# Performance work log

Measured on AMD Instinct MI355X. Metric: run time of the kernel, lower is better.

## Reference

```python
import jax, jax.numpy as jnp
import numpy as np

N, E = 4096, 131072
IN_DIM, HID, OUT_DIM = 128, 64, 128
H1 = 4                       # gat1 heads
D_MODEL = HID * H1           # 256
NHEAD = 4
D_FF = 2048


def setup_inputs() -> dict:
    key = jax.random.key(0)
    ks = jax.random.split(key, 16)
    def w(k, shape, scale=0.05):
        return jax.random.normal(k, shape, dtype=jnp.float32) * scale
    return {
        "x": jax.random.normal(ks[0], (N, IN_DIM), dtype=jnp.float32),
        "edge_index": jax.random.randint(ks[1], (2, E), 0, N, dtype=jnp.int32),
        "gat1_w": w(ks[2], (H1 * HID, IN_DIM)),
        "gat1_asrc": w(ks[3], (H1, HID)),
        "gat1_adst": w(ks[4], (H1, HID)),
        "gat1_b": jnp.zeros((H1 * HID,), jnp.float32),
        "in_proj_w": w(ks[5], (3 * D_MODEL, D_MODEL)),
        "in_proj_b": jnp.zeros((3 * D_MODEL,), jnp.float32),
        "out_proj_w": w(ks[6], (D_MODEL, D_MODEL)),
        "out_proj_b": jnp.zeros((D_MODEL,), jnp.float32),
        "lin1_w": w(ks[7], (D_FF, D_MODEL)),
        "lin1_b": jnp.zeros((D_FF,), jnp.float32),
        "lin2_w": w(ks[8], (D_MODEL, D_FF)),
        "lin2_b": jnp.zeros((D_MODEL,), jnp.float32),
        "ln1_g": jnp.ones((D_MODEL,), jnp.float32),
        "ln1_b": jnp.zeros((D_MODEL,), jnp.float32),
        "ln2_g": jnp.ones((D_MODEL,), jnp.float32),
        "ln2_b": jnp.zeros((D_MODEL,), jnp.float32),
        "gat2_w": w(ks[9], (OUT_DIM, D_MODEL)),
        "gat2_asrc": w(ks[10], (1, OUT_DIM)),
        "gat2_adst": w(ks[11], (1, OUT_DIM)),
        "gat2_b": jnp.zeros((OUT_DIM,), jnp.float32),
    }


def _add_self_loops(ei, n):
    loops = jnp.arange(n, dtype=ei.dtype)
    return jnp.concatenate([ei, jnp.stack([loops, loops])], axis=1)


def _segment_softmax(logits, seg, n):
    # numerically stable softmax over edges grouped by destination node
    m = jax.ops.segment_max(logits, seg, num_segments=n)
    m = jnp.where(jnp.isfinite(m), m, 0.0)
    e = jnp.exp(logits - m[seg])
    s = jax.ops.segment_sum(e, seg, num_segments=n)
    return e / (s[seg] + 1e-16)


def _gat(x, ei, W, asrc, adst, b, heads, out_ch):
    n = x.shape[0]
    h = (x @ W.T).reshape(n, heads, out_ch)          # [N,H,C]
    al_s = jnp.einsum('nhc,hc->nh', h, asrc)
    al_d = jnp.einsum('nhc,hc->nh', h, adst)
    src, dst = ei[0], ei[1]
    logits = jax.nn.leaky_relu(al_s[src] + al_d[dst], 0.2)   # [E,H]
    alpha = _segment_softmax(logits, dst, n)
    out = jax.ops.segment_sum(h[src] * alpha[:, :, None], dst, num_segments=n)
    return out.reshape(n, heads * out_ch) + b


def _ln(x, g, b):
    mu = x.mean(-1, keepdims=True)
    v = x.var(-1, keepdims=True)
    return (x - mu) / jnp.sqrt(v + 1e-5) * g + b


def _forward(x, edge_index, gat1_w, gat1_asrc, gat1_adst, gat1_b,
             in_proj_w, in_proj_b, out_proj_w, out_proj_b,
             lin1_w, lin1_b, lin2_w, lin2_b, ln1_g, ln1_b, ln2_g, ln2_b,
             gat2_w, gat2_asrc, gat2_adst, gat2_b):
    n = x.shape[0]
    ei = _add_self_loops(edge_index, n)
    h = jax.nn.elu(_gat(x, ei, gat1_w, gat1_asrc, gat1_adst, gat1_b, H1, HID))  # [N, 256]
    # TransformerEncoderLayer (post-norm, relu, no dropout in eval)
    hd = D_MODEL // NHEAD
    qkv = h @ in_proj_w.T + in_proj_b
    q, k, v = jnp.split(qkv, 3, axis=-1)
    q = q.reshape(n, NHEAD, hd)
    k = k.reshape(n, NHEAD, hd)
    v = v.reshape(n, NHEAD, hd)
    scores = jnp.einsum('qhd,khd->hqk', q, k) / jnp.sqrt(jnp.float32(hd))
    attn = jax.nn.softmax(scores, axis=-1)
    o = jnp.einsum('hqk,khd->qhd', attn, v).reshape(n, D_MODEL)
    o = o @ out_proj_w.T + out_proj_b
    h = _ln(h + o, ln1_g, ln1_b)
    ff = jax.nn.relu(h @ lin1_w.T + lin1_b) @ lin2_w.T + lin2_b
    h = _ln(h + ff, ln2_g, ln2_b)
    return _gat(h, ei, gat2_w, gat2_asrc, gat2_adst, gat2_b, 1, OUT_DIM)


def reference(x, edge_index, gat1_w, gat1_asrc, gat1_adst, gat1_b,
              in_proj_w, in_proj_b, out_proj_w, out_proj_b,
              lin1_w, lin1_b, lin2_w, lin2_b, ln1_g, ln1_b, ln2_g, ln2_b,
              gat2_w, gat2_asrc, gat2_adst, gat2_b):
    return _forward(x, edge_index, gat1_w, gat1_asrc, gat1_adst, gat1_b,
                    in_proj_w, in_proj_b, out_proj_w, out_proj_b,
                    lin1_w, lin1_b, lin2_w, lin2_b, ln1_g, ln1_b, ln2_g, ln2_b,
                    gat2_w, gat2_asrc, gat2_adst, gat2_b)
```

## Files before the change

kernel.cpp:

```cpp
#include <hip/hip_runtime.h>
#include <hip/hip_bf16.h>
#include <math.h>

#define NN 4096
#define NE 131072
#define EE (NE + NN)

typedef unsigned short u16;
typedef short s8v __attribute__((ext_vector_type(8)));
typedef float f4v __attribute__((ext_vector_type(4)));
typedef float f16v __attribute__((ext_vector_type(16)));

__device__ inline u16 f2b(float f) {
  __hip_bfloat16 h = __float2bfloat16(f);
  return __builtin_bit_cast(u16, h);
}
__device__ inline float b2f(u16 v) {
  unsigned int u = ((unsigned int)v) << 16;
  return __builtin_bit_cast(float, u);
}

__global__ void k_count(const int* __restrict__ ei, int* __restrict__ deg) {
  int e = blockIdx.x * 256 + threadIdx.x;
  if (e >= EE) return;
  int dst = (e < NE) ? ei[NE + e] : (e - NE);
  atomicAdd(&deg[dst], 1);
}

__global__ __launch_bounds__(1024) void k_scan(const int* __restrict__ deg, int* __restrict__ rowptr) {
  __shared__ int lds[1024];
  int t = threadIdx.x;
  int v0 = deg[t*4+0], v1 = deg[t*4+1], v2 = deg[t*4+2], v3 = deg[t*4+3];
  int s1 = v0+v1, s2 = s1+v2, s3 = s2+v3;
  lds[t] = s3;
  __syncthreads();
  for (int off = 1; off < 1024; off <<= 1) {
    int add = (t >= off) ? lds[t-off] : 0;
    __syncthreads();
    lds[t] += add;
    __syncthreads();
  }
  int base = lds[t] - s3;
  rowptr[t*4+1] = base + v0;
  rowptr[t*4+2] = base + s1;
  rowptr[t*4+3] = base + s2;
  rowptr[t*4+4] = base + s3;
  if (t == 0) rowptr[0] = 0;
}

__global__ void k_scatter(const int* __restrict__ ei, const int* __restrict__ rowptr,
                          int* __restrict__ cursor, int* __restrict__ csr_src) {
  int e = blockIdx.x * 256 + threadIdx.x;
  if (e >= EE) return;
  int src, dst;
  if (e < NE) { src = ei[e]; dst = ei[NE + e]; }
  else { src = e - NE; dst = src; }
  int pos = rowptr[dst] + atomicAdd(&cursor[dst], 1);
  csr_src[pos] = src;
}

__global__ __launch_bounds__(256) void k_f2b_all(
    const float* a0, u16* b0, int e0, const float* a1, u16* b1, int e1,
    const float* a2, u16* b2, int e2, const float* a3, u16* b3, int e3,
    const float* a4, u16* b4, int e4, const float* a5, u16* b5, int e5,
    const float* a6, u16* b6, int e6)
{
  int i = blockIdx.x * 256 + threadIdx.x;
  const float* s; u16* d; int base;
  if      (i < e0) { s=a0; d=b0; base=0;  }
  else if (i < e1) { s=a1; d=b1; base=e0; }
  else if (i < e2) { s=a2; d=b2; base=e1; }
  else if (i < e3) { s=a3; d=b3; base=e2; }
  else if (i < e4) { s=a4; d=b4; base=e3; }
  else if (i < e5) { s=a5; d=b5; base=e4; }
  else if (i < e6) { s=a6; d=b6; base=e5; }
  else return;
  int j = i - base;
  float4 v = ((const float4*)s)[j];
  u16 r[4] = {f2b(v.x), f2b(v.y), f2b(v.z), f2b(v.w)};
  *(uint2*)(d + (size_t)j*4) = *(uint2*)r;
}

template<int HEADS, int C>
__global__ __launch_bounds__(256) void k_alogits(
    const u16* __restrict__ featb, const float* __restrict__ asrc,
    const float* __restrict__ adst, float* __restrict__ als, float* __restrict__ ald)
{
  constexpr int F = HEADS * C;
  int n = blockIdx.x, t = threadIdx.x;
  float f = b2f(featb[(size_t)n*F + t]);
  float ps = f * asrc[t];
  float pd = f * adst[t];
  #pragma unroll
  for (int off = 32; off; off >>= 1) {
    ps += __shfl_xor(ps, off);
    pd += __shfl_xor(pd, off);
  }
  if constexpr (C == 64) {
    if ((t & 63) == 0) {
      int hh = t >> 6;
      als[(size_t)n*HEADS + hh] = ps;
      ald[(size_t)n*HEADS + hh] = pd;
    }
  } else {
    __shared__ float sh[2][2];
    if ((t & 63) == 0) { sh[t>>6][0] = ps; sh[t>>6][1] = pd; }
    __syncthreads();
    if (t == 0) {
      als[n] = sh[0][0] + sh[1][0];
      ald[n] = sh[0][1] + sh[1][1];
    }
  }
}

template<int HEADS, int C, bool DO_ELU, bool WB>
__global__ __launch_bounds__(256) void k_gat_agg(
    const u16* __restrict__ featb, const float* __restrict__ als,
    const float* __restrict__ ald, const float* __restrict__ bias,
    const int* __restrict__ rowptr, const int* __restrict__ csr_src,
    float* __restrict__ out, u16* __restrict__ outb)
{
  constexpr int F = HEADS * C;
  int n = blockIdx.x, t = threadIdx.x;
  __shared__ float m_sh[HEADS], s_sh[HEADS];
  __shared__ float alpha_sh[HEADS][64];
  __shared__ int src_sh[64];
  int start = rowptr[n];
  int deg = rowptr[n+1] - start;
  int lane = t & 63, wv = t >> 6;
  for (int hh = wv; hh < HEADS; hh += F/64) {
    float adl = ald[(size_t)n*HEADS + hh];
    float mx = -INFINITY;
    for (int i = lane; i < deg; i += 64) {
      int s = csr_src[start + i];
      float lg = als[(size_t)s*HEADS + hh] + adl;
      lg = (lg > 0.f) ? lg : 0.2f * lg;
      mx = fmaxf(mx, lg);
    }
    #pragma unroll
    for (int off = 32; off; off >>= 1) mx = fmaxf(mx, __shfl_xor(mx, off));
    float sm = 0.f;
    for (int i = lane; i < deg; i += 64) {
      int s = csr_src[start + i];
      float lg = als[(size_t)s*HEADS + hh] + adl;
      lg = (lg > 0.f) ? lg : 0.2f * lg;
      sm += expf(lg - mx);
    }
    #pragma unroll
    for (int off = 32; off; off >>= 1) sm += __shfl_xor(sm, off);
    if (lane == 0) { m_sh[hh] = mx; s_sh[hh] = sm; }
  }
  __syncthreads();
  int hh = t / C;
  int hh2 = t >> 6;
  int ia = t & 63;
  float acc0 = 0.f, acc1 = 0.f;
  for (int c0 = 0; c0 < deg; c0 += 64) {
    int cn = min(64, deg - c0);
    if (hh2 < HEADS && ia < cn) {
      int s = csr_src[start + c0 + ia];
      if (hh2 == 0) src_sh[ia] = s;
      float lg = als[(size_t)s*HEADS + hh2] + ald[(size_t)n*HEADS + hh2];
      lg = (lg > 0.f) ? lg : 0.2f * lg;
      alpha_sh[hh2][ia] = expf(lg - m_sh[hh2]);
    }
    __syncthreads();
    int i = 0;
    for (; i + 1 < cn; i += 2) {
      int s0 = src_sh[i], s1 = src_sh[i+1];
      float a0 = alpha_sh[hh][i], a1 = alpha_sh[hh][i+1];
      acc0 += a0 * b2f(featb[(size_t)s0*F + t]);
      acc1 += a1 * b2f(featb[(size_t)s1*F + t]);
    }
    if (i < cn)
      acc0 += alpha_sh[hh][i] * b2f(featb[(size_t)src_sh[i]*F + t]);
    __syncthreads();
  }
  float o = (acc0 + acc1) / (s_sh[hh] + 1e-16f) + bias[t];
  if (DO_ELU) o = (o > 0.f) ? o : (expf(o) - 1.f);
  out[(size_t)n*F + t] = o;
  if (WB) outb[(size_t)n*F + t] = f2b(o);
}

template<int MODE>
__global__ __launch_bounds__(256) void k_gemm_mfma(
    const u16* __restrict__ A, const u16* __restrict__ B,
    const float* __restrict__ bias, float* __restrict__ Cf, u16* __restrict__ Cb,
    u16* __restrict__ Qb, u16* __restrict__ Kb, u16* __restrict__ Vt,
    int M, int N, int K)
{
  __shared__ u16 Al[64*64];
  __shared__ u16 Bl[64*64];
  char* Ab = (char*)Al;
  char* Bb = (char*)Bl;
  const int t = threadIdx.x;
  const int lane = t & 63;
  const int lr = lane & 15, lk = lane >> 4;
  const int wid = t >> 6;
  const int wm = wid & 1, wn = wid >> 1;
  const int m0 = blockIdx.y * 64, n0 = blockIdx.x * 64;

  f4v acc[2][2];
  #pragma unroll
  for (int mi = 0; mi < 2; ++mi)
    #pragma unroll
    for (int ni = 0; ni < 2; ++ni)
      acc[mi][ni] = f4v{0.f, 0.f, 0.f, 0.f};

  for (int k0 = 0; k0 < K; k0 += 64) {
    #pragma unroll
    for (int i = 0; i < 2; ++i) {
      int idx = t + i*256;
      int row = idx >> 3, ch = idx & 7;
      s8v av = *(const s8v*)(A + (size_t)(m0 + row)*K + k0 + ch*8);
      *(s8v*)(Ab + row*128 + ((ch*16) ^ ((row & 7) << 4))) = av;
      s8v bv = *(const s8v*)(B + (size_t)(n0 + row)*K + k0 + ch*8);
      *(s8v*)(Bb + row*128 + ((ch*16) ^ ((row & 7) << 4))) = bv;
    }
    __syncthreads();
    #pragma unroll
    for (int ks = 0; ks < 2; ++ks) {
      s8v af[2], bfr[2];
      #pragma unroll
      for (int mi = 0; mi < 2; ++mi) {
        int row = wm*32 + mi*16 + lr;
        int ch = ks*4 + lk;
        af[mi] = *(const s8v*)(Ab + row*128 + ((ch*16) ^ ((row & 7) << 4)));
      }
      #pragma unroll
      for (int ni = 0; ni < 2; ++ni) {
        int row = wn*32 + ni*16 + lr;
        int ch = ks*4 + lk;
        bfr[ni] = *(const s8v*)(Bb + row*128 + ((ch*16) ^ ((row & 7) << 4)));
      }
      #pragma unroll
      for (int mi = 0; mi < 2; ++mi)
        #pragma unroll
        for (int ni = 0; ni < 2; ++ni)
          acc[mi][ni] = __builtin_amdgcn_mfma_f32_16x16x32_bf16(af[mi], bfr[ni], acc[mi][ni], 0, 0, 0);
    }
    __syncthreads();
  }
  #pragma unroll
  for (int ni = 0; ni < 2; ++ni) {
    int col = n0 + wn*32 + ni*16 + lr;
    float bc = bias ? bias[col] : 0.f;
    #pragma unroll
    for (int mi = 0; mi < 2; ++mi) {
      int row0 = m0 + wm*32 + mi*16 + lk*4;
      float v[4];
      #pragma unroll
      for (int r = 0; r < 4; ++r) v[r] = acc[mi][ni][r] + bc;
      if (MODE == 0) {
        #pragma unroll
        for (int r = 0; r < 4; ++r) Cf[(size_t)(row0 + r)*N + col] = v[r];
      } else if (MODE == 2) {
        #pragma unroll
        for (int r = 0; r < 4; ++r) Cb[(size_t)(row0 + r)*N + col] = f2b(v[r]);
      } else {
        if (col < 512) {
          int head = (col >> 6) & 3;
          int d = col & 63;
          u16* dst = ((col < 256) ? Qb : Kb) + (size_t)head*262144 + d;
          #pragma unroll
          for (int r = 0; r < 4; ++r) dst[(size_t)(row0 + r)*64] = f2b(v[r]);
        } else {
          int cc = col - 512;
          int head = cc >> 6;
          int d = cc & 63;
          int quad = row0 & 12;
          int qs = (quad == 4) ? 8 : ((quad == 8) ? 4 : quad);
          size_t nphys = (size_t)((row0 & ~15) | qs);
          u16 o4[4];
          #pragma unroll
          for (int r = 0; r < 4; ++r) o4[r] = f2b(v[r]);
          *(uint2*)(Vt + (size_t)head*262144 + (size_t)d*4096 + nphys) = *(uint2*)o4;
        }
      }
    }
  }
}

template<int MODE>
__global__ __launch_bounds__(256) void k_gemm2(
    const u16* __restrict__ A, const u16* __restrict__ B,
    const float* __restrict__ bias, float* __restrict__ Cf, u16* __restrict__ Cb,
    int M, int N, int K, int ksl)
{
  __shared__ u16 Al[128*64];
  __shared__ u16 Bl[64*64];
  char* Ab = (char*)Al;
  char* Bb = (char*)Bl;
  const int t = threadIdx.x;
  const int lane = t & 63;
  const int lr = lane & 15, lk = lane >> 4;
  const int wv = t >> 6;
  const int m0 = blockIdx.y * 128, n0 = blockIdx.x * 64;
  const int z = blockIdx.z;
  const int kbeg = z * ksl, kend = kbeg + ksl;

  f4v acc[2][4];
  #pragma unroll
  for (int mi = 0; mi < 2; ++mi)
    #pragma unroll
    for (int ni = 0; ni < 4; ++ni)
      acc[mi][ni] = f4v{0.f, 0.f, 0.f, 0.f};

  for (int k0 = kbeg; k0 < kend; k0 += 64) {
    #pragma unroll
    for (int i = 0; i < 4; ++i) {
      int idx = t + i*256;
      int row = idx >> 3, ch = idx & 7;
      s8v av = *(const s8v*)(A + (size_t)(m0 + row)*K + k0 + ch*8);
      *(s8v*)(Ab + row*128 + ((ch*16) ^ ((row & 7) << 4))) = av;
    }
    #pragma unroll
    for (int i = 0; i < 2; ++i) {
      int idx = t + i*256;
      int row = idx >> 3, ch = idx & 7;
      s8v bv = *(const s8v*)(B + (size_t)(n0 + row)*K + k0 + ch*8);
      *(s8v*)(Bb + row*128 + ((ch*16) ^ ((row & 7) << 4))) = bv;
    }
    __syncthreads();
    #pragma unroll
    for (int ks = 0; ks < 2; ++ks) {
      s8v af[2], bfr[4];
      #pragma unroll
      for (int mi = 0; mi < 2; ++mi) {
        int row = wv*32 + mi*16 + lr;
        int ch = ks*4 + lk;
        af[mi] = *(const s8v*)(Ab + row*128 + ((ch*16) ^ ((row & 7) << 4)));
      }
      #pragma unroll
      for (int ni = 0; ni < 4; ++ni) {
        int row = ni*16 + lr;
        int ch = ks*4 + lk;
        bfr[ni] = *(const s8v*)(Bb + row*128 + ((ch*16) ^ ((row & 7) << 4)));
      }
      #pragma unroll
      for (int mi = 0; mi < 2; ++mi)
        #pragma unroll
        for (int ni = 0; ni < 4; ++ni)
          acc[mi][ni] = __builtin_amdgcn_mfma_f32_16x16x32_bf16(af[mi], bfr[ni], acc[mi][ni], 0, 0, 0);
    }
    __syncthreads();
  }
  #pragma unroll
  for (int ni = 0; ni < 4; ++ni) {
    int col = n0 + ni*16 + lr;
    float bc = (MODE == 4) ? 0.f : bias[col];
    #pragma unroll
    for (int mi = 0; mi < 2; ++mi) {
      int row0 = m0 + wv*32 + mi*16 + lk*4;
      #pragma unroll
      for (int r = 0; r < 4; ++r) {
        float v = acc[mi][ni][r] + bc;
        if (MODE == 1) {
          v = fmaxf(v, 0.f);
          Cb[(size_t)(row0 + r)*N + col] = f2b(v);
        } else {
          (Cf + (size_t)z*M*N)[(size_t)(row0 + r)*N + col] = v;
        }
      }
    }
  }
}

template<bool WB>
__global__ __launch_bounds__(256) void k_ln(
    const float* __restrict__ a, const float* __restrict__ res,
    const float* __restrict__ g, const float* __restrict__ bb,
    float* __restrict__ out, u16* __restrict__ outb)
{
  int n = blockIdx.x, t = threadIdx.x;
  __shared__ float part[4];
  float v = a[(size_t)n*256 + t] + res[(size_t)n*256 + t];
  float s = v;
  #pragma unroll
  for (int off = 32; off; off >>= 1) s += __shfl_xor(s, off);
  if ((t & 63) == 0) part[t >> 6] = s;
  __syncthreads();
  float mean = (part[0] + part[1] + part[2] + part[3]) * (1.f/256.f);
  __syncthreads();
  float d = v - mean;
  float s2 = d * d;
  #pragma unroll
  for (int off = 32; off; off >>= 1) s2 += __shfl_xor(s2, off);
  if ((t & 63) == 0) part[t >> 6] = s2;
  __syncthreads();
  float var = (part[0] + part[1] + part[2] + part[3]) * (1.f/256.f);
  float rstd = rsqrtf(var + 1e-5f);
  float o = d * rstd * g[t] + bb[t];
  out[(size_t)n*256 + t] = o;
  if (WB) outb[(size_t)n*256 + t] = f2b(o);
}

template<bool WB>
__global__ __launch_bounds__(256) void k_ln_sk(
    const float* __restrict__ Po, const float* __restrict__ bias,
    const float* __restrict__ res, const float* __restrict__ g,
    const float* __restrict__ bb, float* __restrict__ out, u16* __restrict__ outb)
{
  int n = blockIdx.x, t = threadIdx.x;
  __shared__ float part[4];
  const size_t MN = (size_t)NN * 256;
  size_t idx = (size_t)n*256 + t;
  float v = Po[idx] + Po[MN + idx] + Po[2*MN + idx] + Po[3*MN + idx]
          + bias[t] + res[idx];
  float s = v;
  #pragma unroll
  for (int off = 32; off; off >>= 1) s += __shfl_xor(s, off);
  if ((t & 63) == 0) part[t >> 6] = s;
  __syncthreads();
  float mean = (part[0] + part[1] + part[2] + part[3]) * (1.f/256.f);
  __syncthreads();
  float d = v - mean;
  float s2 = d * d;
  #pragma unroll
  for (int off = 32; off; off >>= 1) s2 += __shfl_xor(s2, off);
  if ((t & 63) == 0) part[t >> 6] = s2;
  __syncthreads();
  float var = (part[0] + part[1] + part[2] + part[3]) * (1.f/256.f);
  float rstd = rsqrtf(var + 1e-5f);
  float o = d * rstd * g[t] + bb[t];
  out[idx] = o;
  if (WB) outb[idx] = f2b(o);
}

__global__ __launch_bounds__(512) void k_attn2(
    const u16* __restrict__ Qb, const u16* __restrict__ Kb,
    const u16* __restrict__ Vt, float* __restrict__ op,
    float* __restrict__ mb, float* __restrict__ lb)
{
  const int strip = blockIdx.x;
  const int head  = blockIdx.y;
  const int z     = blockIdx.z;
  const int q0 = strip * 32;
  const int t = threadIdx.x;
  const int s = t >> 6;
  const int l = t & 63;
  const int lq = l & 31;
  const int lh = l >> 5;

  __shared__ float lds_O[4][32][68];
  __shared__ float lds_m[4][32];
  __shared__ float lds_l[4][32];

  const u16* Qh = Qb + (size_t)head * (4096*64);
  const u16* Kh = Kb + (size_t)head * (4096*64);
  const u16* Vh = Vt + (size_t)head * (64*4096);

  s8v qf[4];
#pragma unroll
  for (int dc = 0; dc < 4; ++dc)
    qf[dc] = *(const s8v*)(Qh + (size_t)(q0 + lq)*64 + dc*16 + lh*8);

  f16v accO[2];
#pragma unroll
  for (int dm = 0; dm < 2; ++dm)
#pragma unroll
    for (int i = 0; i < 16; ++i) accO[dm][i] = 0.f;

  float mrow = -INFINITY, lrow = 0.f;
  const float CE = 0.18033688011112042f;

  const int kt0 = z * 2048 + s * 256;
  for (int kt = kt0; kt < kt0 + 256; kt += 64) {
    f16v st[2];
#pragma unroll
    for (int c = 0; c < 2; ++c)
#pragma unroll
      for (int i = 0; i < 16; ++i) st[c][i] = 0.f;
#pragma unroll
    for (int dc = 0; dc < 4; ++dc) {
      s8v kf0 = *(const s8v*)(Kh + (size_t)(kt + lq)*64 + dc*16 + lh*8);
      s8v kf1 = *(const s8v*)(Kh + (size_t)(kt + 32 + lq)*64 + dc*16 + lh*8);
      st[0] = __builtin_amdgcn_mfma_f32_32x32x16_bf16(kf0, qf[dc], st[0], 0, 0, 0);
      st[1] = __builtin_amdgcn_mfma_f32_32x32x16_bf16(kf1, qf[dc], st[1], 0, 0, 0);
    }
    float mx = st[0][0];
#pragma unroll
    for (int i = 1; i < 16; ++i) mx = fmaxf(mx, st[0][i]);
#pragma unroll
    for (int i = 0; i < 16; ++i) mx = fmaxf(mx, st[1][i]);
    mx = fmaxf(mx, __shfl_xor(mx, 32));
    float mn = fmaxf(mrow, mx);
    float sc = exp2f((mrow - mn) * CE);
    mrow = mn;
    float ps = 0.f;
#pragma unroll
    for (int c = 0; c < 2; ++c)
#pragma unroll
      for (int i = 0; i < 16; ++i) {
        float p = exp2f((st[c][i] - mn) * CE);
        st[c][i] = p;
        ps += p;
      }
    ps += __shfl_xor(ps, 32);
    lrow = lrow * sc + ps;
#pragma unroll
    for (int dm = 0; dm < 2; ++dm)
#pragma unroll
      for (int i = 0; i < 16; ++i) accO[dm][i] *= sc;

#pragma unroll
    for (int c = 0; c < 2; ++c) {
#pragma unroll
      for (int kc = 0; kc < 2; ++kc) {
        union { s8v v; unsigned int w[4]; } pb;
#pragma unroll
        for (int wd = 0; wd < 4; ++wd) {
          u16 lo16 = f2b(st[c][kc*8 + wd*2]);
          u16 hi16 = f2b(st[c][kc*8 + wd*2 + 1]);
          pb.w[wd] = (unsigned int)lo16 | ((unsigned int)hi16 << 16);
        }
#pragma unroll
        for (int dm = 0; dm < 2; ++dm) {
          s8v vf = *(const s8v*)(Vh + (size_t)(dm*32 + lq)*4096 + kt + c*32 + kc*16 + lh*8);
          accO[dm] = __builtin_amdgcn_mfma_f32_32x32x16_bf16(vf, pb.v, accO[dm], 0, 0, 0);
        }
      }
    }
  }

#pragma unroll
  for (int lev = 0; lev < 3; ++lev) {
    const int step = 1 << lev;
    __syncthreads();
    if ((s & (2*step - 1)) == step) {
      int slot = (s - step) >> (lev + 1);
      if (l < 32) { lds_m[slot][lq] = mrow; lds_l[slot][lq] = lrow; }
#pragma unroll
      for (int dm = 0; dm < 2; ++dm)
#pragma unroll
        for (int g = 0; g < 4; ++g) {
          f4v v;
#pragma unroll
          for (int rr = 0; rr < 4; ++rr) v[rr] = accO[dm][g*4 + rr];
          *(f4v*)&lds_O[slot][lq][dm*32 + lh*4 + g*8] = v;
        }
    }
    __syncthreads();
    if ((s & (2*step - 1)) == 0) {
      int slot = s >> (lev + 1);
      float mp = lds_m[slot][lq], lp = lds_l[slot][lq];
      float M = fmaxf(mrow, mp);
      float w0 = exp2f((mrow - M) * CE);
      float w1 = exp2f((mp - M) * CE);
      lrow = lrow * w0 + lp * w1;
      mrow = M;
#pragma unroll
      for (int dm = 0; dm < 2; ++dm)
#pragma unroll
        for (int g = 0; g < 4; ++g) {
          f4v vp = *(const f4v*)&lds_O[slot][lq][dm*32 + lh*4 + g*8];
#pragma unroll
          for (int rr = 0; rr < 4; ++rr)
            accO[dm][g*4 + rr] = accO[dm][g*4 + rr] * w0 + vp[rr] * w1;
        }
    }
  }

  if (s == 0) {
    int pb = (z*4 + head)*128 + strip;
    if (l < 32) { mb[pb*32 + lq] = mrow; lb[pb*32 + lq] = lrow; }
#pragma unroll
    for (int dm = 0; dm < 2; ++dm)
#pragma unroll
      for (int g = 0; g < 4; ++g) {
        f4v v;
#pragma unroll
        for (int rr = 0; rr < 4; ++rr) v[rr] = accO[dm][g*4 + rr];
        *(f4v*)&op[(size_t)pb*2048 + lq*64 + dm*32 + lh*4 + g*8] = v;
      }
  }
}

__global__ __launch_bounds__(256) void k_attn_mrg(
    const float* __restrict__ op, const float* __restrict__ mb,
    const float* __restrict__ lb, u16* __restrict__ attno_b)
{
  const int strip = blockIdx.x;
  const int head = blockIdx.y;
  const int t = threadIdx.x;
  const int q = t >> 3;
  const int d0 = (t & 7) * 8;
  const float CE = 0.18033688011112042f;
  int p0 = (0*4 + head)*128 + strip;
  int p1 = (1*4 + head)*128 + strip;
  float m0 = mb[p0*32 + q], m1 = mb[p1*32 + q];
  float M = fmaxf(m0, m1);
  float w0 = exp2f((m0 - M) * CE);
  float w1 = exp2f((m1 - M) * CE);
  float L = w0 * lb[p0*32 + q] + w1 * lb[p1*32 + q];
  float inv = 1.f / L;
  const float* o0 = op + (size_t)p0*2048 + q*64 + d0;
  const float* o1 = op + (size_t)p1*2048 + q*64 + d0;
  u16 o8[8];
#pragma unroll
  for (int i = 0; i < 8; ++i)
    o8[i] = f2b((w0 * o0[i] + w1 * o1[i]) * inv);
  *(uint4*)(attno_b + (size_t)(strip*32 + q)*256 + head*64 + d0) = *(uint4*)o8;
}

extern "C" void kernel_launch(void* const* d_in, const int* in_sizes, int n_in,
                              void* d_out, int out_size, void* d_ws, size_t ws_size,
                              hipStream_t stream)
{
  const float* x       = (const float*)d_in[0];
  const int*   ei      = (const int*)d_in[1];
  const float* gat1_w  = (const float*)d_in[2];
  const float* gat1_as = (const float*)d_in[3];
  const float* gat1_ad = (const float*)d_in[4];
  const float* gat1_b  = (const float*)d_in[5];
  const float* inp_w   = (const float*)d_in[6];
  const float* inp_b   = (const float*)d_in[7];
  const float* outp_w  = (const float*)d_in[8];
  const float* outp_b  = (const float*)d_in[9];
  const float* lin1_w  = (const float*)d_in[10];
  const float* lin1_b  = (const float*)d_in[11];
  const float* lin2_w  = (const float*)d_in[12];
  const float* lin2_b  = (const float*)d_in[13];
  const float* ln1_g   = (const float*)d_in[14];
  const float* ln1_bb  = (const float*)d_in[15];
  const float* ln2_g   = (const float*)d_in[16];
  const float* ln2_bb  = (const float*)d_in[17];
  const float* gat2_w  = (const float*)d_in[18];
  const float* gat2_as = (const float*)d_in[19];
  const float* gat2_ad = (const float*)d_in[20];
  const float* gat2_b  = (const float*)d_in[21];
  float* out = (float*)d_out;
  (void)in_sizes; (void)n_in; (void)out_size; (void)ws_size;

  char* ws = (char*)d_ws;
  size_t off = 0;
  auto nxt = [&](size_t bytes) { size_t r = off; off += (bytes + 255) & ~(size_t)255; return r; };
  int* deg      = (int*)(ws + nxt((size_t)NN*4));
  int* cursor   = (int*)(ws + nxt((size_t)NN*4));
  int* rowptr   = (int*)(ws + nxt((size_t)(NN+1)*4));
  int* csr_src  = (int*)(ws + nxt((size_t)EE*4));
  float* al1s   = (float*)(ws + nxt((size_t)NN*4*4));
  float* al1d   = (float*)(ws + nxt((size_t)NN*4*4));
  float* hgat1  = (float*)(ws + nxt((size_t)NN*256*4));
  float* tmp256 = (float*)(ws + nxt((size_t)NN*256*4));
  float* hln1   = (float*)(ws + nxt((size_t)NN*256*4));
  float* hln2   = (float*)(ws + nxt((size_t)NN*256*4));
  float* Po     = (float*)(ws + nxt((size_t)4*NN*256*4));
  float* al2s   = (float*)(ws + nxt((size_t)NN*4));
  float* al2d   = (float*)(ws + nxt((size_t)NN*4));
  u16* x_b      = (u16*)(ws + nxt((size_t)NN*128*2));
  u16* feat1_b  = (u16*)(ws + nxt((size_t)NN*256*2));
  u16* feat2_b  = (u16*)(ws + nxt((size_t)NN*128*2));
  u16* hgat1_b  = (u16*)(ws + nxt((size_t)NN*256*2));
  u16* attno_b  = (u16*)(ws + nxt((size_t)NN*256*2));
  u16* hln1_b   = (u16*)(ws + nxt((size_t)NN*256*2));
  u16* hln2_b   = (u16*)(ws + nxt((size_t)NN*256*2));
  u16* ff1_b    = (u16*)(ws + nxt((size_t)NN*2048*2));
  u16* Qb       = (u16*)(ws + nxt((size_t)4*4096*64*2));
  u16* Kb       = (u16*)(ws + nxt((size_t)4*4096*64*2));
  u16* Vt       = (u16*)(ws + nxt((size_t)4*4096*64*2));
  u16* inp_w_b  = (u16*)(ws + nxt((size_t)768*256*2));
  u16* outp_w_b = (u16*)(ws + nxt((size_t)256*256*2));
  u16* lin1_w_b = (u16*)(ws + nxt((size_t)2048*256*2));
  u16* lin2_w_b = (u16*)(ws + nxt((size_t)256*2048*2));
  u16* gat1_w_b = (u16*)(ws + nxt((size_t)256*128*2));
  u16* gat2_w_b = (u16*)(ws + nxt((size_t)128*256*2));

  float* a_op = Po;
  float* a_mb = Po + (size_t)1024*2048;
  float* a_lb = a_mb + 32768;

  hipMemsetAsync(deg, 0, (size_t)NN*4, stream);
  hipMemsetAsync(cursor, 0, (size_t)NN*4, stream);
  k_count<<<(EE+255)/256, 256, 0, stream>>>(ei, deg);
  k_scan<<<1, 1024, 0, stream>>>(deg, rowptr);
  k_scatter<<<(EE+255)/256, 256, 0, stream>>>(ei, rowptr, cursor, csr_src);

  k_f2b_all<<<1856, 256, 0, stream>>>(
      inp_w,  inp_w_b,  49152,
      outp_w, outp_w_b, 65536,
      lin1_w, lin1_w_b, 196608,
      lin2_w, lin2_w_b, 327680,
      gat1_w, gat1_w_b, 335872,
      gat2_w, gat2_w_b, 344064,
      x,      x_b,      475136);

  k_gemm_mfma<2><<<dim3(4, 64), 256, 0, stream>>>(x_b, gat1_w_b, nullptr, nullptr, feat1_b, nullptr, nullptr, nullptr, NN, 256, 128);
  k_alogits<4,64><<<NN, 256, 0, stream>>>(feat1_b, gat1_as, gat1_ad, al1s, al1d);
  k_gat_agg<4,64,true,true><<<NN, 256, 0, stream>>>(feat1_b, al1s, al1d, gat1_b, rowptr, csr_src, hgat1, hgat1_b);

  k_gemm_mfma<3><<<dim3(12, 64), 256, 0, stream>>>(hgat1_b, inp_w_b, inp_b, nullptr, nullptr, Qb, Kb, Vt, NN, 768, 256);
  k_attn2<<<dim3(128, 4, 2), 512, 0, stream>>>(Qb, Kb, Vt, a_op, a_mb, a_lb);
  k_attn_mrg<<<dim3(128, 4), 256, 0, stream>>>(a_op, a_mb, a_lb, attno_b);
  k_gemm_mfma<0><<<dim3(4, 64), 256, 0, stream>>>(attno_b, outp_w_b, outp_b, tmp256, nullptr, nullptr, nullptr, nullptr, NN, 256, 256);
  k_ln<true><<<NN, 256, 0, stream>>>(tmp256, hgat1, ln1_g, ln1_bb, hln1, hln1_b);
  k_gemm2<1><<<dim3(32, 32), 256, 0, stream>>>(hln1_b, lin1_w_b, lin1_b, nullptr, ff1_b, NN, 2048, 256, 256);
  k_gemm2<4><<<dim3(4, 32, 4), 256, 0, stream>>>(ff1_b, lin2_w_b, nullptr, Po, nullptr, NN, 256, 2048, 512);
  k_ln_sk<true><<<NN, 256, 0, stream>>>(Po, lin2_b, hln1, ln2_g, ln2_bb, hln2, hln2_b);

  k_gemm_mfma<2><<<dim3(2, 64), 256, 0, stream>>>(hln2_b, gat2_w_b, nullptr, nullptr, feat2_b, nullptr, nullptr, nullptr, NN, 128, 256);
  k_alogits<1,128><<<NN, 128, 0, stream>>>(feat2_b, gat2_as, gat2_ad, al2s, al2d);
  k_gat_agg<1,128,false,false><<<NN, 128, 0, stream>>>(feat2_b, al2s, al2d, gat2_b, rowptr, csr_src, out, nullptr);
}
```

Baseline: 300.1 us.

## Share K/V tiles in LDS across query waves and split keys eight ways

Rewrites the attention kernel so four waves working on different query strips share swizzled K/V tiles staged in LDS, with register prefetch of the next tile. The key range is split into eight chunks across the grid instead of two plus an in-block tree reduction, and a new merge kernel combines eight partial softmax states. This cuts redundant global K/V loads per wave and removes the intra-block reduction. In exchange it writes and reads larger partial output buffers, reusing the ff1 buffer as scratch.

```diff
diff --git a/kernel.cpp b/kernel.cpp
--- a/kernel.cpp
+++ b/kernel.cpp
@@ -427,24 +427,25 @@
   if (WB) outb[idx] = f2b(o);
 }
 
-__global__ __launch_bounds__(512) void k_attn2(
+__global__ __launch_bounds__(256) void k_attn3(
     const u16* __restrict__ Qb, const u16* __restrict__ Kb,
-    const u16* __restrict__ Vt, float* __restrict__ op,
-    float* __restrict__ mb, float* __restrict__ lb)
+    const u16* __restrict__ Vt, float* __restrict__ op0, float* __restrict__ op1,
+    float* __restrict__ mball, float* __restrict__ lball)
 {
   const int strip = blockIdx.x;
   const int head  = blockIdx.y;
   const int z     = blockIdx.z;
-  const int q0 = strip * 32;
   const int t = threadIdx.x;
-  const int s = t >> 6;
+  const int wv = t >> 6;
   const int l = t & 63;
   const int lq = l & 31;
   const int lh = l >> 5;
-
-  __shared__ float lds_O[4][32][68];
-  __shared__ float lds_m[4][32];
-  __shared__ float lds_l[4][32];
+  const int q0 = strip*128 + wv*32;
+
+  __shared__ u16 Kl[64*64];
+  __shared__ u16 Vl[64*64];
+  char* Kc = (char*)Kl;
+  char* Vc = (char*)Vl;
 
   const u16* Qh = Qb + (size_t)head * (4096*64);
   const u16* Kh = Kb + (size_t)head * (4096*64);
@@ -455,17 +456,65 @@
   for (int dc = 0; dc < 4; ++dc)
     qf[dc] = *(const s8v*)(Qh + (size_t)(q0 + lq)*64 + dc*16 + lh*8);
 
+  const int c0 = t, c1 = t + 256;
+  const int kr0 = c0 >> 3, kc0 = c0 & 7;
+  const int kr1 = c1 >> 3, kc1 = c1 & 7;
+  const int kt0 = z * 512;
+  const u16* gK0 = Kh + (size_t)(kt0 + kr0)*64 + kc0*8;
+  const u16* gK1 = Kh + (size_t)(kt0 + kr1)*64 + kc1*8;
+  const u16* gV0 = Vh + (size_t)kr0*4096 + kt0 + kc0*8;
+  const u16* gV1 = Vh + (size_t)kr1*4096 + kt0 + kc1*8;
+  const int lo0 = kr0*128 + ((kc0*16) ^ ((kr0 & 7) << 4));
+  const int lo1 = kr1*128 + ((kc1*16) ^ ((kr1 & 7) << 4));
+
+  {
+    s8v a = *(const s8v*)gK0, b = *(const s8v*)gK1;
+    s8v c = *(const s8v*)gV0, d = *(const s8v*)gV1;
+    *(s8v*)(Kc + lo0) = a; *(s8v*)(Kc + lo1) = b;
+    *(s8v*)(Vc + lo0) = c; *(s8v*)(Vc + lo1) = d;
+  }
+  __syncthreads();
+
+  int roK[2][4];
+#pragma unroll
+  for (int c = 0; c < 2; ++c) {
+    int row = c*32 + lq;
+#pragma unroll
+    for (int dc = 0; dc < 4; ++dc)
+      roK[c][dc] = row*128 + ((dc*32 + lh*16) ^ ((row & 7) << 4));
+  }
+  int roV[2][2][2];
+#pragma unroll
+  for (int dm = 0; dm < 2; ++dm) {
+    int row = dm*32 + lq;
+#pragma unroll
+    for (int c = 0; c < 2; ++c)
+#pragma unroll
+      for (int kc = 0; kc < 2; ++kc)
+        roV[c][kc][dm] = row*128 + ((c*64 + kc*32 + lh*16) ^ ((row & 7) << 4));
+  }
+
   f16v accO[2];
 #pragma unroll
   for (int dm = 0; dm < 2; ++dm)
 #pragma unroll
     for (int i = 0; i < 16; ++i) accO[dm][i] = 0.f;
-
   float mrow = -INFINITY, lrow = 0.f;
   const float CE = 0.18033688011112042f;
 
-  const int kt0 = z * 2048 + s * 256;
-  for (int kt = kt0; kt < kt0 + 256; kt += 64) {
+  s8v rK0, rK1, rV0, rV1;
+  for (int tt = 0; tt < 8; ++tt) {
+    if (tt < 7) {
+      gK0 += 64*64; gK1 += 64*64; gV0 += 64; gV1 += 64;
+      rK0 = *(const s8v*)gK0; rK1 = *(const s8v*)gK1;
+      rV0 = *(const s8v*)gV0; rV1 = *(const s8v*)gV1;
+    }
+    s8v kf[2][4];
+#pragma unroll
+    for (int c = 0; c < 2; ++c)
+#pragma unroll
+      for (int dc = 0; dc < 4; ++dc)
+        kf[c][dc] = *(const s8v*)(Kc + roK[c][dc]);
     f16v st[2];
 #pragma unroll
     for (int c = 0; c < 2; ++c)
@@ -473,10 +522,8 @@
       for (int i = 0; i < 16; ++i) st[c][i] = 0.f;
 #pragma unroll
     for (int dc = 0; dc < 4; ++dc) {
-      s8v kf0 = *(const s8v*)(Kh + (size_t)(kt + lq)*64 + dc*16 + lh*8);
-      s8v kf1 = *(const s8v*)(Kh + (size_t)(kt + 32 + lq)*64 + dc*16 + lh*8);
-      st[0] = __builtin_amdgcn_mfma_f32_32x32x16_bf16(kf0, qf[dc], st[0], 0, 0, 0);
-      st[1] = __builtin_amdgcn_mfma_f32_32x32x16_bf16(kf1, qf[dc], st[1], 0, 0, 0);
+      st[0] = __builtin_amdgcn_mfma_f32_32x32x16_bf16(kf[0][dc], qf[dc], st[0], 0, 0, 0);
+      st[1] = __builtin_amdgcn_mfma_f32_32x32x16_bf16(kf[1][dc], qf[dc], st[1], 0, 0, 0);
     }
     float mx = st[0][0];
 #pragma unroll
@@ -507,6 +554,8 @@
     for (int c = 0; c < 2; ++c) {
 #pragma unroll
       for (int kc = 0; kc < 2; ++kc) {
+        s8v vf0 = *(const s8v*)(Vc + roV[c][kc][0]);
+        s8v vf1 = *(const s8v*)(Vc + roV[c][kc][1]);
         union { s8v v; unsigned int w[4]; } pb;
 #pragma unroll
         for (int wd = 0; wd < 4; ++wd) {
@@ -514,93 +563,72 @@
           u16 hi16 = f2b(st[c][kc*8 + wd*2 + 1]);
           pb.w[wd] = (unsigned int)lo16 | ((unsigned int)hi16 << 16);
         }
-#pragma unroll
-        for (int dm = 0; dm < 2; ++dm) {
-          s8v vf = *(const s8v*)(Vh + (size_t)(dm*32 + lq)*4096 + kt + c*32 + kc*16 + lh*8);
-          accO[dm] = __builtin_amdgcn_mfma_f32_32x32x16_bf16(vf, pb.v, accO[dm], 0, 0, 0);
-        }
+        accO[0] = __builtin_amdgcn_mfma_f32_32x32x16_bf16(vf0, pb.v, accO[0], 0, 0, 0);
+        accO[1] = __builtin_amdgcn_mfma_f32_32x32x16_bf16(vf1, pb.v, accO[1], 0, 0, 0);
       }
     }
-  }
-
-#pragma unroll
-  for (int lev = 0; lev < 3; ++lev) {
-    const int step = 1 << lev;
-    __syncthreads();
-    if ((s & (2*step - 1)) == step) {
-      int slot = (s - step) >> (lev + 1);
-      if (l < 32) { lds_m[slot][lq] = mrow; lds_l[slot][lq] = lrow; }
-#pragma unroll
-      for (int dm = 0; dm < 2; ++dm)
-#pragma unroll
-        for (int g = 0; g < 4; ++g) {
-          f4v v;
-#pragma unroll
-          for (int rr = 0; rr < 4; ++rr) v[rr] = accO[dm][g*4 + rr];
-          *(f4v*)&lds_O[slot][lq][dm*32 + lh*4 + g*8] = v;
-        }
-    }
-    __syncthreads();
-    if ((s & (2*step - 1)) == 0) {
-      int slot = s >> (lev + 1);
-      float mp = lds_m[slot][lq], lp = lds_l[slot][lq];
-      float M = fmaxf(mrow, mp);
-      float w0 = exp2f((mrow - M) * CE);
-      float w1 = exp2f((mp - M) * CE);
-      lrow = lrow * w0 + lp * w1;
-      mrow = M;
-#pragma unroll
-      for (int dm = 0; dm < 2; ++dm)
-#pragma unroll
-        for (int g = 0; g < 4; ++g) {
-          f4v vp = *(const f4v*)&lds_O[slot][lq][dm*32 + lh*4 + g*8];
-#pragma unroll
-          for (int rr = 0; rr < 4; ++rr)
-            accO[dm][g*4 + rr] = accO[dm][g*4 + rr] * w0 + vp[rr] * w1;
-        }
-    }
-  }
-
-  if (s == 0) {
-    int pb = (z*4 + head)*128 + strip;
-    if (l < 32) { mb[pb*32 + lq] = mrow; lb[pb*32 + lq] = lrow; }
-#pragma unroll
-    for (int dm = 0; dm < 2; ++dm)
-#pragma unroll
-      for (int g = 0; g < 4; ++g) {
-        f4v v;
-#pragma unroll
-        for (int rr = 0; rr < 4; ++rr) v[rr] = accO[dm][g*4 + rr];
-        *(f4v*)&op[(size_t)pb*2048 + lq*64 + dm*32 + lh*4 + g*8] = v;
-      }
-  }
-}
-
-__global__ __launch_bounds__(256) void k_attn_mrg(
-    const float* __restrict__ op, const float* __restrict__ mb,
-    const float* __restrict__ lb, u16* __restrict__ attno_b)
-{
-  const int strip = blockIdx.x;
+    __syncthreads();
+    if (tt < 7) {
+      *(s8v*)(Kc + lo0) = rK0; *(s8v*)(Kc + lo1) = rK1;
+      *(s8v*)(Vc + lo0) = rV0; *(s8v*)(Vc + lo1) = rV1;
+      __syncthreads();
+    }
+  }
+
+  int q = q0 + lq;
+  int pidx = (z*4 + head)*4096 + q;
+  if (lh == 0) { mball[pidx] = mrow; lball[pidx] = lrow; }
+  float* op = (z < 4) ? op0 : op1;
+  size_t obase = ((size_t)((z & 3)*4 + head)*4096 + q)*64;
+#pragma unroll
+  for (int dm = 0; dm < 2; ++dm)
+#pragma unroll
+    for (int g = 0; g < 4; ++g) {
+      f4v v;
+#pragma unroll
+      for (int rr = 0; rr < 4; ++rr) v[rr] = accO[dm][g*4 + rr];
+      *(f4v*)&op[obase + dm*32 + lh*4 + g*8] = v;
+    }
+}
+
+__global__ __launch_bounds__(256) void k_attn_mrg8(
+    const float* __restrict__ op0, const float* __restrict__ op1,
+    const float* __restrict__ mball, const float* __restrict__ lball,
+    u16* __restrict__ attno_b)
+{
+  const int bq = blockIdx.x;
   const int head = blockIdx.y;
   const int t = threadIdx.x;
-  const int q = t >> 3;
+  const int q = bq*32 + (t >> 3);
   const int d0 = (t & 7) * 8;
   const float CE = 0.18033688011112042f;
-  int p0 = (0*4 + head)*128 + strip;
-  int p1 = (1*4 + head)*128 + strip;
-  float m0 = mb[p0*32 + q], m1 = mb[p1*32 + q];
-  float M = fmaxf(m0, m1);
-  float w0 = exp2f((m0 - M) * CE);
-  float w1 = exp2f((m1 - M) * CE);
-  float L = w0 * lb[p0*32 + q] + w1 * lb[p1*32 + q];
+  float m[8], M = -INFINITY;
+#pragma unroll
+  for (int z = 0; z < 8; ++z) {
+    m[z] = mball[(z*4 + head)*4096 + q];
+    M = fmaxf(M, m[z]);
+  }
+  float w[8], L = 0.f;
+#pragma unroll
+  for (int z = 0; z < 8; ++z) {
+    w[z] = exp2f((m[z] - M) * CE);
+    L += w[z] * lball[(z*4 + head)*4096 + q];
+  }
   float inv = 1.f / L;
-  const float* o0 = op + (size_t)p0*2048 + q*64 + d0;
-  const float* o1 = op + (size_t)p1*2048 + q*64 + d0;
+  float o[8] = {0,0,0,0,0,0,0,0};
+#pragma unroll
+  for (int z = 0; z < 8; ++z) {
+    const float* op = (z < 4) ? op0 : op1;
+    size_t base = ((size_t)((z & 3)*4 + head)*4096 + q)*64 + d0;
+    f4v a = *(const f4v*)&op[base];
+    f4v b = *(const f4v*)&op[base + 4];
+#pragma unroll
+    for (int i = 0; i < 4; ++i) { o[i] += w[z]*a[i]; o[4+i] += w[z]*b[i]; }
+  }
   u16 o8[8];
 #pragma unroll
-  for (int i = 0; i < 8; ++i)
-    o8[i] = f2b((w0 * o0[i] + w1 * o1[i]) * inv);
-  *(uint4*)(attno_b + (size_t)(strip*32 + q)*256 + head*64 + d0) = *(uint4*)o8;
+  for (int i = 0; i < 8; ++i) o8[i] = f2b(o[i] * inv);
+  *(uint4*)(attno_b + (size_t)q*256 + head*64 + d0) = *(uint4*)o8;
 }
 
 extern "C" void kernel_launch(void* const* d_in, const int* in_sizes, int n_in,
@@ -648,6 +676,8 @@
   float* Po     = (float*)(ws + nxt((size_t)4*NN*256*4));
   float* al2s   = (float*)(ws + nxt((size_t)NN*4));
   float* al2d   = (float*)(ws + nxt((size_t)NN*4));
+  float* mball  = (float*)(ws + nxt((size_t)32*NN*4));
+  float* lball  = (float*)(ws + nxt((size_t)32*NN*4));
   u16* x_b      = (u16*)(ws + nxt((size_t)NN*128*2));
   u16* feat1_b  = (u16*)(ws + nxt((size_t)NN*256*2));
   u16* feat2_b  = (u16*)(ws + nxt((size_t)NN*128*2));
@@ -666,9 +696,8 @@
   u16* gat1_w_b = (u16*)(ws + nxt((size_t)256*128*2));
   u16* gat2_w_b = (u16*)(ws + nxt((size_t)128*256*2));
 
-  float* a_op = Po;
-  float* a_mb = Po + (size_t)1024*2048;
-  float* a_lb = a_mb + 32768;
+  float* op0 = Po;
+  float* op1 = (float*)ff1_b;
 
   hipMemsetAsync(deg, 0, (size_t)NN*4, stream);
   hipMemsetAsync(cursor, 0, (size_t)NN*4, stream);
@@ -690,8 +719,8 @@
   k_gat_agg<4,64,true,true><<<NN, 256, 0, stream>>>(feat1_b, al1s, al1d, gat1_b, rowptr, csr_src, hgat1, hgat1_b);
 
   k_gemm_mfma<3><<<dim3(12, 64), 256, 0, stream>>>(hgat1_b, inp_w_b, inp_b, nullptr, nullptr, Qb, Kb, Vt, NN, 768, 256);
-  k_attn2<<<dim3(128, 4, 2), 512, 0, stream>>>(Qb, Kb, Vt, a_op, a_mb, a_lb);
-  k_attn_mrg<<<dim3(128, 4), 256, 0, stream>>>(a_op, a_mb, a_lb, attno_b);
+  k_attn3<<<dim3(32, 4, 8), 256, 0, stream>>>(Qb, Kb, Vt, op0, op1, mball, lball);
+  k_attn_mrg8<<<dim3(128, 4), 256, 0, stream>>>(op0, op1, mball, lball, attno_b);
   k_gemm_mfma<0><<<dim3(4, 64), 256, 0, stream>>>(attno_b, outp_w_b, outp_b, tmp256, nullptr, nullptr, nullptr, nullptr, NN, 256, 256);
   k_ln<true><<<NN, 256, 0, stream>>>(tmp256, hgat1, ln1_g, ln1_bb, hln1, hln1_b);
   k_gemm2<1><<<dim3(32, 32), 256, 0, stream>>>(hln1_b, lin1_w_b, lin1_b, nullptr, ff1_b, NN, 2048, 256, 256);
```

Measured after the change: 275.0 us. -8.3%, faster.
